# Kernel optimization log

Measured on AMD Instinct MI355X. Metric: run time of the kernel, lower is better.

## Reference

```python
import jax, jax.numpy as jnp
import numpy as np

N, DEG, F = 500000, 16, 128
H1, H2, OUT = 256, 256, 128


def setup_inputs() -> dict:
    key = jax.random.key(0)
    ks = jax.random.split(key, 8)
    s = lambda fan_in: 1.0 / np.sqrt(fan_in)
    return {
        "message": jax.random.normal(ks[0], (N, DEG, F), dtype=jnp.float32),
        "features": jax.random.normal(ks[1], (N, F), dtype=jnp.float32),
        "global_features": jax.random.normal(ks[2], (N, F), dtype=jnp.float32),
        "W1": jax.random.normal(ks[3], (3 * F, H1), dtype=jnp.float32) * s(3 * F),
        "b1": jnp.zeros((H1,), dtype=jnp.float32),
        "W2": jax.random.normal(ks[4], (H1, H2), dtype=jnp.float32) * s(H1),
        "b2": jnp.zeros((H2,), dtype=jnp.float32),
        "W3": jax.random.normal(ks[5], (H2, OUT), dtype=jnp.float32) * s(H2),
        "b3": jnp.zeros((OUT,), dtype=jnp.float32),
    }


def reference(message, features, global_features, W1, b1, W2, b2, W3, b3):
    # mailbox sum-aggregate over neighbors: [N, deg, F] -> [N, F]
    agg = jnp.sum(message, axis=1)
    # concat aggregated messages with node + global features: [N, 3F]
    x = jnp.concatenate([agg, features, global_features], axis=1)
    # MLP: Linear+ReLU, Linear+ReLU, Linear
    h = jax.nn.relu(x @ W1 + b1)
    h = jax.nn.relu(h @ W2 + b2)
    out = h @ W3 + b3
    # row-wise L2 (Frobenius over dim=1) normalization
    norm = jnp.linalg.norm(out, axis=1, keepdims=True)
    return out / (norm + 1e-8)
```

## Files before the change

kernel.cpp:

```cpp
#include <hip/hip_runtime.h>


typedef short short8   __attribute__((ext_vector_type(8)));
typedef short short4_t __attribute__((ext_vector_type(4)));
typedef float f32x4    __attribute__((ext_vector_type(4)));

#define SWZ(row, off) ((off) ^ (((row) & 7) << 4))

__device__ __forceinline__ unsigned short f2bf(float f) {
    unsigned int u = __float_as_uint(f);
    u += 0x7fffu + ((u >> 16) & 1u);
    return (unsigned short)(u >> 16);
}

__global__ void prep_weights(const float* __restrict__ W1,
                             const float* __restrict__ W2,
                             const float* __restrict__ W3,
                             short* __restrict__ pw1,
                             short* __restrict__ pw2,
                             short* __restrict__ pw3) {
    int idx = blockIdx.x * 256 + threadIdx.x;
    if (idx < 98304) {
        int j = idx & 7, l = (idx >> 3) & 63, g = idx >> 9;
        int ks = g % 12, tn = g / 12;
        int n = tn * 16 + (l & 15);
        int k = ks * 32 + ((l >> 4) << 3) + j;
        pw1[idx] = (short)f2bf(W1[k * 256 + n]);
    } else if (idx < 98304 + 65536) {
        int e = idx - 98304;
        int j = e & 7, l = (e >> 3) & 63, g = e >> 9;
        int ks = g & 7, tn = g >> 3;
        int n = tn * 16 + (l & 15);
        int k = ks * 32 + ((l >> 4) << 3) + j;
        pw2[e] = (short)f2bf(W2[k * 256 + n]);
    } else if (idx < 98304 + 65536 + 32768) {
        int e = idx - 98304 - 65536;
        int j = e & 7, l = (e >> 3) & 63, g = e >> 9;
        int ks = g & 7, tn = g >> 3;
        int n = tn * 16 + (l & 15);
        int k = ks * 32 + ((l >> 4) << 3) + j;
        pw3[e] = (short)f2bf(W3[k * 128 + n]);
    }
}

__global__ __launch_bounds__(256, 4) void node_net(
    const float* __restrict__ msg,
    const float* __restrict__ feat,
    const float* __restrict__ glob,
    const float* __restrict__ b1v,
    const float* __restrict__ b2v,
    const float* __restrict__ b3v,
    const short* __restrict__ pw1,
    const short* __restrict__ pw2,
    const short* __restrict__ pw3,
    float* __restrict__ out,
    int n_rows)
{
    __shared__ char lds[32768];
    char* regA = lds;
    char* regB = lds + 16384;

    const int tid  = threadIdx.x;
    const int lane = tid & 63;
    const int w    = tid >> 6;
    const int lr   = lane & 15;
    const int lk   = lane >> 4;
    const long long r0 = (long long)blockIdx.x * 32;

    const f32x4 zero4 = {0.f, 0.f, 0.f, 0.f};

    f32x4 acc1[2][4];
    #pragma unroll
    for (int ri = 0; ri < 2; ++ri)
        #pragma unroll
        for (int ci = 0; ci < 4; ++ci) acc1[ri][ci] = zero4;

    #pragma unroll
    for (int p = 0; p < 3; ++p) {
        if (p == 0) {
            #pragma unroll
            for (int pass = 0; pass < 2; ++pass) {
                const int f4 = tid & 31;
                const int rA = (tid >> 5) + pass * 16;
                const int rB = rA + 8;
                const long long rowA = r0 + rA, rowB = r0 + rB;
                f32x4 a = zero4, b = zero4;
                const f32x4* mpA = (const f32x4*)msg + rowA * 512 + f4;
                const f32x4* mpB = (const f32x4*)msg + rowB * 512 + f4;
                if (rowB < n_rows) {
                    #pragma unroll
                    for (int d = 0; d < 16; ++d) { a += mpA[d * 32]; b += mpB[d * 32]; }
                } else if (rowA < n_rows) {
                    #pragma unroll
                    for (int d = 0; d < 16; ++d) { a += mpA[d * 32]; }
                }
                short4_t sa, sb;
                sa[0] = (short)f2bf(a[0]); sa[1] = (short)f2bf(a[1]);
                sa[2] = (short)f2bf(a[2]); sa[3] = (short)f2bf(a[3]);
                sb[0] = (short)f2bf(b[0]); sb[1] = (short)f2bf(b[1]);
                sb[2] = (short)f2bf(b[2]); sb[3] = (short)f2bf(b[3]);
                *(short4_t*)(regB + SWZ(rA, rA * 256 + f4 * 8)) = sa;
                *(short4_t*)(regB + SWZ(rB, rB * 256 + f4 * 8)) = sb;
            }
        } else {
            const f32x4* sp = (const f32x4*)(p == 1 ? feat : glob);
            #pragma unroll
            for (int pass = 0; pass < 4; ++pass) {
                const int f4 = tid & 31;
                const int r  = (tid >> 5) + pass * 8;
                const long long row = r0 + r;
                f32x4 a = zero4;
                if (row < n_rows) a = sp[row * 32 + f4];
                short4_t s4;
                s4[0] = (short)f2bf(a[0]); s4[1] = (short)f2bf(a[1]);
                s4[2] = (short)f2bf(a[2]); s4[3] = (short)f2bf(a[3]);
                *(short4_t*)(regB + SWZ(r, r * 256 + f4 * 8)) = s4;
            }
        }
        __syncthreads();

        #pragma unroll
        for (int s = 0; s < 4; ++s) {
            const int ks = p * 4 + s;
            short8 a[2], b[4];
            #pragma unroll
            for (int ri = 0; ri < 2; ++ri) {
                int row = ri * 16 + lr;
                int off = row * 256 + s * 64 + lk * 16;
                a[ri] = *(const short8*)(regB + SWZ(row, off));
            }
            #pragma unroll
            for (int ci = 0; ci < 4; ++ci) {
                int tn = w * 4 + ci;
                b[ci] = *(const short8*)(pw1 + (((tn * 12 + ks) * 64 + lane) << 3));
            }
            #pragma unroll
            for (int ri = 0; ri < 2; ++ri)
                #pragma unroll
                for (int ci = 0; ci < 4; ++ci)
                    acc1[ri][ci] = __builtin_amdgcn_mfma_f32_16x16x32_bf16(
                        a[ri], b[ci], acc1[ri][ci], 0, 0, 0);
        }
        __syncthreads();
    }

    #pragma unroll
    for (int ci = 0; ci < 4; ++ci) {
        int col = w * 64 + ci * 16 + lr;
        float bias = b1v[col];
        #pragma unroll
        for (int ri = 0; ri < 2; ++ri)
            #pragma unroll
            for (int i = 0; i < 4; ++i) {
                int row = ri * 16 + lk * 4 + i;
                float v = fmaxf(acc1[ri][ci][i] + bias, 0.f);
                int off = row * 512 + col * 2;
                *(short*)(regA + SWZ(row, off)) = (short)f2bf(v);
            }
    }
    __syncthreads();

    f32x4 acc2[2][4];
    #pragma unroll
    for (int ri = 0; ri < 2; ++ri)
        #pragma unroll
        for (int ci = 0; ci < 4; ++ci) acc2[ri][ci] = zero4;

    #pragma unroll
    for (int s = 0; s < 8; ++s) {
        short8 a[2], b[4];
        #pragma unroll
        for (int ri = 0; ri < 2; ++ri) {
            int row = ri * 16 + lr;
            int off = row * 512 + s * 64 + lk * 16;
            a[ri] = *(const short8*)(regA + SWZ(row, off));
        }
        #pragma unroll
        for (int ci = 0; ci < 4; ++ci) {
            int tn = w * 4 + ci;
            b[ci] = *(const short8*)(pw2 + (((tn * 8 + s) * 64 + lane) << 3));
        }
        #pragma unroll
        for (int ri = 0; ri < 2; ++ri)
            #pragma unroll
            for (int ci = 0; ci < 4; ++ci)
                acc2[ri][ci] = __builtin_amdgcn_mfma_f32_16x16x32_bf16(
                    a[ri], b[ci], acc2[ri][ci], 0, 0, 0);
    }

    #pragma unroll
    for (int ci = 0; ci < 4; ++ci) {
        int col = w * 64 + ci * 16 + lr;
        float bias = b2v[col];
        #pragma unroll
        for (int ri = 0; ri < 2; ++ri)
            #pragma unroll
            for (int i = 0; i < 4; ++i) {
                int row = ri * 16 + lk * 4 + i;
                float v = fmaxf(acc2[ri][ci][i] + bias, 0.f);
                int off = row * 512 + col * 2;
                *(short*)(regB + SWZ(row, off)) = (short)f2bf(v);
            }
    }
    __syncthreads();

    f32x4 acc3[2][2];
    #pragma unroll
    for (int ri = 0; ri < 2; ++ri)
        #pragma unroll
        for (int ci = 0; ci < 2; ++ci) acc3[ri][ci] = zero4;

    #pragma unroll
    for (int s = 0; s < 8; ++s) {
        short8 a[2], b[2];
        #pragma unroll
        for (int ri = 0; ri < 2; ++ri) {
            int row = ri * 16 + lr;
            int off = row * 512 + s * 64 + lk * 16;
            a[ri] = *(const short8*)(regB + SWZ(row, off));
        }
        #pragma unroll
        for (int ci = 0; ci < 2; ++ci) {
            int tn = w * 2 + ci;
            b[ci] = *(const short8*)(pw3 + (((tn * 8 + s) * 64 + lane) << 3));
        }
        #pragma unroll
        for (int ri = 0; ri < 2; ++ri)
            #pragma unroll
            for (int ci = 0; ci < 2; ++ci)
                acc3[ri][ci] = __builtin_amdgcn_mfma_f32_16x16x32_bf16(
                    a[ri], b[ci], acc3[ri][ci], 0, 0, 0);
    }

    #pragma unroll
    for (int ci = 0; ci < 2; ++ci) {
        int col = w * 32 + ci * 16 + lr;
        float bias = b3v[col];
        #pragma unroll
        for (int ri = 0; ri < 2; ++ri)
            #pragma unroll
            for (int i = 0; i < 4; ++i) {
                int row = ri * 16 + lk * 4 + i;
                float v = acc3[ri][ci][i] + bias;
                int off = row * 512 + col * 4;
                *(float*)(regA + SWZ(row, off)) = v;
            }
    }
    __syncthreads();

    #pragma unroll
    for (int pass = 0; pass < 4; ++pass) {
        const int r  = (tid >> 5) + pass * 8;
        const int fl = tid & 31;
        int off = r * 512 + fl * 16;
        f32x4 v = *(const f32x4*)(regA + SWZ(r, off));
        float ss = v[0]*v[0] + v[1]*v[1] + v[2]*v[2] + v[3]*v[3];
        ss += __shfl_xor(ss, 1, 32);
        ss += __shfl_xor(ss, 2, 32);
        ss += __shfl_xor(ss, 4, 32);
        ss += __shfl_xor(ss, 8, 32);
        ss += __shfl_xor(ss, 16, 32);
        float inv = 1.f / (sqrtf(ss) + 1e-8f);
        long long row = r0 + r;
        if (row < n_rows) {
            f32x4 o = v * inv;
            ((f32x4*)out)[row * 32 + fl] = o;
        }
    }
}

extern "C" void kernel_launch(void* const* d_in, const int* in_sizes, int n_in,
                              void* d_out, int out_size, void* d_ws, size_t ws_size,
                              hipStream_t stream) {
    const float* msg  = (const float*)d_in[0];
    const float* feat = (const float*)d_in[1];
    const float* glob = (const float*)d_in[2];
    const float* W1   = (const float*)d_in[3];
    const float* b1   = (const float*)d_in[4];
    const float* W2   = (const float*)d_in[5];
    const float* b2   = (const float*)d_in[6];
    const float* W3   = (const float*)d_in[7];
    const float* b3   = (const float*)d_in[8];
    float* out = (float*)d_out;

    const int n_rows = in_sizes[1] / 128;

    short* pw1 = (short*)d_ws;
    short* pw2 = pw1 + 98304;
    short* pw3 = pw2 + 65536;

    hipLaunchKernelGGL(prep_weights, dim3(768), dim3(256), 0, stream,
                       W1, W2, W3, pw1, pw2, pw3);

    const int nblocks = (n_rows + 31) / 32;
    hipLaunchKernelGGL(node_net, dim3(nblocks), dim3(256), 0, stream,
                       msg, feat, glob, b1, b2, b3, pw1, pw2, pw3, out, n_rows);
}
```

Baseline: 1.285 ms.

## Restructure node MLP into single-wave blocks of 16 nodes with weights as MFMA A-operand

Replaces the 256-thread, 32-row block with a 64-thread single-wave block handling 16 nodes. The weights become the A operand so each wave computes all output columns, which removes the __syncthreads barriers. Features are loaded straight into registers, and the row norm is reduced in registers. It also adds nontemporal loads and stores for the streaming message, feature and output data. The trade-off is that each wave now reads the full weight set for only 16 nodes, which raises weight traffic through L2/L1, and each wave holds larger accumulator arrays, which raises register pressure.

New measurement: 1.475 ms. +14.7%, slower.

```diff
diff --git a/kernel.cpp b/kernel.cpp
--- a/kernel.cpp
+++ b/kernel.cpp
@@ -43,7 +43,7 @@
     }
 }
 
-__global__ __launch_bounds__(256, 4) void node_net(
+__global__ __launch_bounds__(64, 4) void node_wave(
     const float* __restrict__ msg,
     const float* __restrict__ feat,
     const float* __restrict__ glob,
@@ -56,215 +56,142 @@
     float* __restrict__ out,
     int n_rows)
 {
-    __shared__ char lds[32768];
-    char* regA = lds;
-    char* regB = lds + 16384;
-
-    const int tid  = threadIdx.x;
-    const int lane = tid & 63;
-    const int w    = tid >> 6;
-    const int lr   = lane & 15;
-    const int lk   = lane >> 4;
-    const long long r0 = (long long)blockIdx.x * 32;
-
+    __shared__ char lds[8192];
+
+    const int l    = threadIdx.x;
+    const int node = l & 15;
+    const int lk   = l >> 4;
+    const long long r0 = (long long)blockIdx.x * 16;
     const f32x4 zero4 = {0.f, 0.f, 0.f, 0.f};
 
-    f32x4 acc1[2][4];
-    #pragma unroll
-    for (int ri = 0; ri < 2; ++ri)
-        #pragma unroll
-        for (int ci = 0; ci < 4; ++ci) acc1[ri][ci] = zero4;
-
-    #pragma unroll
-    for (int p = 0; p < 3; ++p) {
-        if (p == 0) {
-            #pragma unroll
-            for (int pass = 0; pass < 2; ++pass) {
-                const int f4 = tid & 31;
-                const int rA = (tid >> 5) + pass * 16;
-                const int rB = rA + 8;
-                const long long rowA = r0 + rA, rowB = r0 + rB;
-                f32x4 a = zero4, b = zero4;
-                const f32x4* mpA = (const f32x4*)msg + rowA * 512 + f4;
-                const f32x4* mpB = (const f32x4*)msg + rowB * 512 + f4;
-                if (rowB < n_rows) {
-                    #pragma unroll
-                    for (int d = 0; d < 16; ++d) { a += mpA[d * 32]; b += mpB[d * 32]; }
-                } else if (rowA < n_rows) {
-                    #pragma unroll
-                    for (int d = 0; d < 16; ++d) { a += mpA[d * 32]; }
-                }
-                short4_t sa, sb;
-                sa[0] = (short)f2bf(a[0]); sa[1] = (short)f2bf(a[1]);
-                sa[2] = (short)f2bf(a[2]); sa[3] = (short)f2bf(a[3]);
-                sb[0] = (short)f2bf(b[0]); sb[1] = (short)f2bf(b[1]);
-                sb[2] = (short)f2bf(b[2]); sb[3] = (short)f2bf(b[3]);
-                *(short4_t*)(regB + SWZ(rA, rA * 256 + f4 * 8)) = sa;
-                *(short4_t*)(regB + SWZ(rB, rB * 256 + f4 * 8)) = sb;
+    #pragma unroll 1
+    for (int c = 0; c < 8; ++c) {
+        const int rA = 2 * c;
+        const long long gA = r0 + rA;
+        const f32x4* base = (const f32x4*)msg + gA * 512;
+        const bool okA = gA < n_rows;
+        const bool okB = (gA + 1) < n_rows;
+        f32x4 tA[8], tB[8];
+        #pragma unroll
+        for (int i = 0; i < 8; ++i)
+            tA[i] = okA ? __builtin_nontemporal_load(base + i * 64 + l) : zero4;
+        #pragma unroll
+        for (int i = 0; i < 8; ++i)
+            tB[i] = okB ? __builtin_nontemporal_load(base + 512 + i * 64 + l) : zero4;
+        f32x4 sA = ((tA[0]+tA[1])+(tA[2]+tA[3])) + ((tA[4]+tA[5])+(tA[6]+tA[7]));
+        f32x4 sB = ((tB[0]+tB[1])+(tB[2]+tB[3])) + ((tB[4]+tB[5])+(tB[6]+tB[7]));
+        #pragma unroll
+        for (int q = 0; q < 4; ++q) {
+            sA[q] += __shfl_xor(sA[q], 32);
+            sB[q] += __shfl_xor(sB[q], 32);
+        }
+        f32x4 s = (l < 32) ? sA : sB;
+        short4_t s4;
+        s4[0] = (short)f2bf(s[0]); s4[1] = (short)f2bf(s[1]);
+        s4[2] = (short)f2bf(s[2]); s4[3] = (short)f2bf(s[3]);
+        const int orow = rA + (l >> 5);
+        *(short4_t*)(lds + SWZ(orow, orow * 256 + (l & 31) * 8)) = s4;
+    }
+
+    f32x4 acc1[16];
+    #pragma unroll
+    for (int m = 0; m < 16; ++m) acc1[m] = zero4;
+
+    #pragma unroll
+    for (int ks = 0; ks < 12; ++ks) {
+        short8 bx;
+        if (ks < 4) {
+            bx = *(const short8*)(lds + SWZ(node, node * 256 + ks * 64 + lk * 16));
+        } else {
+            const float* src = (ks < 8) ? feat : glob;
+            const int kk = (ks < 8) ? (ks - 4) : (ks - 8);
+            const long long row = r0 + node;
+            f32x4 ra = zero4, rb = zero4;
+            if (row < n_rows) {
+                const f32x4* p = (const f32x4*)src + row * 32 + kk * 8 + lk * 2;
+                ra = __builtin_nontemporal_load(p);
+                rb = __builtin_nontemporal_load(p + 1);
             }
-        } else {
-            const f32x4* sp = (const f32x4*)(p == 1 ? feat : glob);
-            #pragma unroll
-            for (int pass = 0; pass < 4; ++pass) {
-                const int f4 = tid & 31;
-                const int r  = (tid >> 5) + pass * 8;
-                const long long row = r0 + r;
-                f32x4 a = zero4;
-                if (row < n_rows) a = sp[row * 32 + f4];
-                short4_t s4;
-                s4[0] = (short)f2bf(a[0]); s4[1] = (short)f2bf(a[1]);
-                s4[2] = (short)f2bf(a[2]); s4[3] = (short)f2bf(a[3]);
-                *(short4_t*)(regB + SWZ(r, r * 256 + f4 * 8)) = s4;
-            }
-        }
-        __syncthreads();
-
-        #pragma unroll
-        for (int s = 0; s < 4; ++s) {
-            const int ks = p * 4 + s;
-            short8 a[2], b[4];
-            #pragma unroll
-            for (int ri = 0; ri < 2; ++ri) {
-                int row = ri * 16 + lr;
-                int off = row * 256 + s * 64 + lk * 16;
-                a[ri] = *(const short8*)(regB + SWZ(row, off));
-            }
-            #pragma unroll
-            for (int ci = 0; ci < 4; ++ci) {
-                int tn = w * 4 + ci;
-                b[ci] = *(const short8*)(pw1 + (((tn * 12 + ks) * 64 + lane) << 3));
-            }
-            #pragma unroll
-            for (int ri = 0; ri < 2; ++ri)
-                #pragma unroll
-                for (int ci = 0; ci < 4; ++ci)
-                    acc1[ri][ci] = __builtin_amdgcn_mfma_f32_16x16x32_bf16(
-                        a[ri], b[ci], acc1[ri][ci], 0, 0, 0);
-        }
-        __syncthreads();
-    }
-
-    #pragma unroll
-    for (int ci = 0; ci < 4; ++ci) {
-        int col = w * 64 + ci * 16 + lr;
-        float bias = b1v[col];
-        #pragma unroll
-        for (int ri = 0; ri < 2; ++ri)
-            #pragma unroll
-            for (int i = 0; i < 4; ++i) {
-                int row = ri * 16 + lk * 4 + i;
-                float v = fmaxf(acc1[ri][ci][i] + bias, 0.f);
-                int off = row * 512 + col * 2;
-                *(short*)(regA + SWZ(row, off)) = (short)f2bf(v);
-            }
-    }
-    __syncthreads();
-
-    f32x4 acc2[2][4];
-    #pragma unroll
-    for (int ri = 0; ri < 2; ++ri)
-        #pragma unroll
-        for (int ci = 0; ci < 4; ++ci) acc2[ri][ci] = zero4;
-
-    #pragma unroll
-    for (int s = 0; s < 8; ++s) {
-        short8 a[2], b[4];
-        #pragma unroll
-        for (int ri = 0; ri < 2; ++ri) {
-            int row = ri * 16 + lr;
-            int off = row * 512 + s * 64 + lk * 16;
-            a[ri] = *(const short8*)(regA + SWZ(row, off));
-        }
-        #pragma unroll
-        for (int ci = 0; ci < 4; ++ci) {
-            int tn = w * 4 + ci;
-            b[ci] = *(const short8*)(pw2 + (((tn * 8 + s) * 64 + lane) << 3));
-        }
-        #pragma unroll
-        for (int ri = 0; ri < 2; ++ri)
-            #pragma unroll
-            for (int ci = 0; ci < 4; ++ci)
-                acc2[ri][ci] = __builtin_amdgcn_mfma_f32_16x16x32_bf16(
-                    a[ri], b[ci], acc2[ri][ci], 0, 0, 0);
-    }
-
-    #pragma unroll
-    for (int ci = 0; ci < 4; ++ci) {
-        int col = w * 64 + ci * 16 + lr;
-        float bias = b2v[col];
-        #pragma unroll
-        for (int ri = 0; ri < 2; ++ri)
-            #pragma unroll
-            for (int i = 0; i < 4; ++i) {
-                int row = ri * 16 + lk * 4 + i;
-                float v = fmaxf(acc2[ri][ci][i] + bias, 0.f);
-                int off = row * 512 + col * 2;
-                *(short*)(regB + SWZ(row, off)) = (short)f2bf(v);
-            }
-    }
-    __syncthreads();
-
-    f32x4 acc3[2][2];
-    #pragma unroll
-    for (int ri = 0; ri < 2; ++ri)
-        #pragma unroll
-        for (int ci = 0; ci < 2; ++ci) acc3[ri][ci] = zero4;
-
-    #pragma unroll
-    for (int s = 0; s < 8; ++s) {
-        short8 a[2], b[2];
-        #pragma unroll
-        for (int ri = 0; ri < 2; ++ri) {
-            int row = ri * 16 + lr;
-            int off = row * 512 + s * 64 + lk * 16;
-            a[ri] = *(const short8*)(regB + SWZ(row, off));
-        }
-        #pragma unroll
-        for (int ci = 0; ci < 2; ++ci) {
-            int tn = w * 2 + ci;
-            b[ci] = *(const short8*)(pw3 + (((tn * 8 + s) * 64 + lane) << 3));
-        }
-        #pragma unroll
-        for (int ri = 0; ri < 2; ++ri)
-            #pragma unroll
-            for (int ci = 0; ci < 2; ++ci)
-                acc3[ri][ci] = __builtin_amdgcn_mfma_f32_16x16x32_bf16(
-                    a[ri], b[ci], acc3[ri][ci], 0, 0, 0);
-    }
-
-    #pragma unroll
-    for (int ci = 0; ci < 2; ++ci) {
-        int col = w * 32 + ci * 16 + lr;
-        float bias = b3v[col];
-        #pragma unroll
-        for (int ri = 0; ri < 2; ++ri)
-            #pragma unroll
-            for (int i = 0; i < 4; ++i) {
-                int row = ri * 16 + lk * 4 + i;
-                float v = acc3[ri][ci][i] + bias;
-                int off = row * 512 + col * 4;
-                *(float*)(regA + SWZ(row, off)) = v;
-            }
-    }
-    __syncthreads();
-
-    #pragma unroll
-    for (int pass = 0; pass < 4; ++pass) {
-        const int r  = (tid >> 5) + pass * 8;
-        const int fl = tid & 31;
-        int off = r * 512 + fl * 16;
-        f32x4 v = *(const f32x4*)(regA + SWZ(r, off));
-        float ss = v[0]*v[0] + v[1]*v[1] + v[2]*v[2] + v[3]*v[3];
-        ss += __shfl_xor(ss, 1, 32);
-        ss += __shfl_xor(ss, 2, 32);
-        ss += __shfl_xor(ss, 4, 32);
-        ss += __shfl_xor(ss, 8, 32);
-        ss += __shfl_xor(ss, 16, 32);
-        float inv = 1.f / (sqrtf(ss) + 1e-8f);
-        long long row = r0 + r;
-        if (row < n_rows) {
-            f32x4 o = v * inv;
-            ((f32x4*)out)[row * 32 + fl] = o;
+            bx[0] = (short)f2bf(ra[0]); bx[1] = (short)f2bf(ra[1]);
+            bx[2] = (short)f2bf(ra[2]); bx[3] = (short)f2bf(ra[3]);
+            bx[4] = (short)f2bf(rb[0]); bx[5] = (short)f2bf(rb[1]);
+            bx[6] = (short)f2bf(rb[2]); bx[7] = (short)f2bf(rb[3]);
+        }
+        #pragma unroll
+        for (int m = 0; m < 16; ++m) {
+            short8 wa = *(const short8*)(pw1 + (((m * 12 + ks) * 64 + l) << 3));
+            acc1[m] = __builtin_amdgcn_mfma_f32_16x16x32_bf16(wa, bx, acc1[m], 0, 0, 0);
+        }
+    }
+
+    #pragma unroll
+    for (int m = 0; m < 16; ++m) {
+        f32x4 b4 = *(const f32x4*)(b1v + m * 16 + lk * 4);
+        short4_t h4;
+        #pragma unroll
+        for (int i = 0; i < 4; ++i)
+            h4[i] = (short)f2bf(fmaxf(acc1[m][i] + b4[i], 0.f));
+        *(short4_t*)(lds + SWZ(node, node * 512 + m * 32 + lk * 8)) = h4;
+    }
+
+    f32x4 acc2[16];
+    #pragma unroll
+    for (int m = 0; m < 16; ++m) acc2[m] = zero4;
+
+    #pragma unroll
+    for (int ks = 0; ks < 8; ++ks) {
+        short8 bx = *(const short8*)(lds + SWZ(node, node * 512 + ks * 64 + lk * 16));
+        #pragma unroll
+        for (int m = 0; m < 16; ++m) {
+            short8 wa = *(const short8*)(pw2 + (((m * 8 + ks) * 64 + l) << 3));
+            acc2[m] = __builtin_amdgcn_mfma_f32_16x16x32_bf16(wa, bx, acc2[m], 0, 0, 0);
+        }
+    }
+
+    #pragma unroll
+    for (int m = 0; m < 16; ++m) {
+        f32x4 b4 = *(const f32x4*)(b2v + m * 16 + lk * 4);
+        short4_t h4;
+        #pragma unroll
+        for (int i = 0; i < 4; ++i)
+            h4[i] = (short)f2bf(fmaxf(acc2[m][i] + b4[i], 0.f));
+        *(short4_t*)(lds + SWZ(node, node * 512 + m * 32 + lk * 8)) = h4;
+    }
+
+    f32x4 acc3[8];
+    #pragma unroll
+    for (int m = 0; m < 8; ++m) acc3[m] = zero4;
+
+    #pragma unroll
+    for (int ks = 0; ks < 8; ++ks) {
+        short8 bx = *(const short8*)(lds + SWZ(node, node * 512 + ks * 64 + lk * 16));
+        #pragma unroll
+        for (int m = 0; m < 8; ++m) {
+            short8 wa = *(const short8*)(pw3 + (((m * 8 + ks) * 64 + l) << 3));
+            acc3[m] = __builtin_amdgcn_mfma_f32_16x16x32_bf16(wa, bx, acc3[m], 0, 0, 0);
+        }
+    }
+
+    float ss = 0.f;
+    #pragma unroll
+    for (int m = 0; m < 8; ++m) {
+        f32x4 b4 = *(const f32x4*)(b3v + m * 16 + lk * 4);
+        #pragma unroll
+        for (int i = 0; i < 4; ++i) {
+            acc3[m][i] += b4[i];
+            ss += acc3[m][i] * acc3[m][i];
+        }
+    }
+    ss += __shfl_xor(ss, 16);
+    ss += __shfl_xor(ss, 32);
+    const float inv = 1.f / (sqrtf(ss) + 1e-8f);
+
+    const long long row = r0 + node;
+    if (row < n_rows) {
+        #pragma unroll
+        for (int m = 0; m < 8; ++m) {
+            f32x4 o = acc3[m] * inv;
+            __builtin_nontemporal_store(o, (f32x4*)out + row * 32 + m * 4 + lk);
         }
     }
 }
@@ -292,7 +219,7 @@
     hipLaunchKernelGGL(prep_weights, dim3(768), dim3(256), 0, stream,
                        W1, W2, W3, pw1, pw2, pw3);
 
-    const int nblocks = (n_rows + 31) / 32;
-    hipLaunchKernelGGL(node_net, dim3(nblocks), dim3(256), 0, stream,
+    const int nblocks = (n_rows + 15) / 16;
+    hipLaunchKernelGGL(node_wave, dim3(nblocks), dim3(64), 0, stream,
                        msg, feat, glob, b1, b2, b3, pw1, pw2, pw3, out, n_rows);
 }
```
